# Performance work log

Hardware: AMD Instinct MI355X
Metric: run time of the kernel (lower is better)

Reference implementation:

```python
import jax, jax.numpy as jnp
import numpy as np
from jax import lax

MID = 64      # mid_size -> token seq len = MID*MID = 4096
DM = 64       # d_model = in_channels
DI = 128      # d_inner = expand * d_model
DS = 16       # d_state
DC = 4        # d_conv
DTR = 4       # dt_rank = ceil(DM/16)
EPS = 1e-5


def conv3x3(x, w):
    return lax.conv_general_dilated(x, w, (1, 1), ((1, 1), (1, 1)),
                                    dimension_numbers=('NCHW', 'OIHW', 'NCHW'))


def layernorm(x, w, b):
    mu = jnp.mean(x, -1, keepdims=True)
    var = jnp.mean((x - mu) ** 2, -1, keepdims=True)
    return (x - mu) * lax.rsqrt(var + EPS) * w + b


def bilinear(x, h, w):
    b, c = x.shape[:2]
    return jax.image.resize(x, (b, c, h, w), method='bilinear', antialias=False)


def mamba(tok, in_w, conv_w, conv_b, xproj_w, dt_w, dt_b, Alog, D, out_w):
    # tok: (b, L, DM)
    b, L, _ = tok.shape
    xz = tok @ in_w.T                                # (b, L, 2*DI)
    xc, z = jnp.split(xz, 2, axis=-1)
    # causal depthwise conv1d over sequence
    xcT = xc.transpose(0, 2, 1)                      # (b, DI, L)
    xconv = lax.conv_general_dilated(xcT, conv_w, (1,), ((DC - 1, 0),),
                                     dimension_numbers=('NCH', 'OIH', 'NCH'),
                                     feature_group_count=DI)
    xconv = xconv + conv_b[None, :, None]
    u = jax.nn.silu(xconv.transpose(0, 2, 1))        # (b, L, DI)
    x_dbl = u @ xproj_w.T                            # (b, L, DTR+2*DS)
    dt, B, C = jnp.split(x_dbl, [DTR, DTR + DS], axis=-1)
    dt = jax.nn.softplus(dt @ dt_w.T + dt_b)         # (b, L, DI)
    A = -jnp.exp(Alog)                               # (DI, DS)
    dA = jnp.exp(dt[..., None] * A)                  # (b, L, DI, DS)
    dBu = dt[..., None] * B[:, :, None, :] * u[..., None]

    def step(h, xs):
        a_t, bu_t = xs
        h = a_t * h + bu_t
        return h, h

    h0 = jnp.zeros((b, DI, DS), dt.dtype)
    _, hs = lax.scan(step, h0, (dA.transpose(1, 0, 2, 3), dBu.transpose(1, 0, 2, 3)))
    y = jnp.einsum('lbns,bls->bln', hs, C) + u * D   # (b, L, DI)
    y = y * jax.nn.silu(z)
    return y @ out_w.T                               # (b, L, DM)


def setup_inputs() -> dict:
    key = jax.random.key(0)
    ks = iter(jax.random.split(key, 32))
    s = 0.02
    d = {}
    d['x'] = jax.random.normal(next(ks), (4, 64, 128, 128), jnp.float32)
    for n, shp in [('cb_w1', (64, 64, 3, 3)), ('cb_w2', (64, 64, 3, 3)),
                   ('sm_w1', (64, 64, 3, 3)), ('sm_w2', (64, 64, 3, 3))]:
        d[n] = jax.random.normal(next(ks), shp, jnp.float32) * s
    d['ln1_w'] = jnp.ones((DM,), jnp.float32); d['ln1_b'] = jnp.zeros((DM,), jnp.float32)
    d['ln2_w'] = jnp.ones((DM,), jnp.float32); d['ln2_b'] = jnp.zeros((DM,), jnp.float32)
    for p in ['m1', 'm2']:
        d[p + '_in_w'] = jax.random.normal(next(ks), (2 * DI, DM), jnp.float32) * s
        d[p + '_conv_w'] = jax.random.normal(next(ks), (DI, 1, DC), jnp.float32) * s
        d[p + '_conv_b'] = jnp.zeros((DI,), jnp.float32)
        d[p + '_xproj_w'] = jax.random.normal(next(ks), (DTR + 2 * DS, DI), jnp.float32) * s
        d[p + '_dt_w'] = jax.random.normal(next(ks), (DI, DTR), jnp.float32) * s
        d[p + '_dt_b'] = jnp.full((DI,), -2.0, jnp.float32)
        d[p + '_Alog'] = jnp.broadcast_to(jnp.log(jnp.arange(1, DS + 1, dtype=jnp.float32)), (DI, DS)).copy()
        d[p + '_D'] = jnp.ones((DI,), jnp.float32)
        d[p + '_out_w'] = jax.random.normal(next(ks), (DM, DI), jnp.float32) * s
    return d


def reference(x, cb_w1, cb_w2, ln1_w, ln1_b, ln2_w, ln2_b,
              m1_in_w, m1_conv_w, m1_conv_b, m1_xproj_w, m1_dt_w, m1_dt_b, m1_Alog, m1_D, m1_out_w,
              m2_in_w, m2_conv_w, m2_conv_b, m2_xproj_w, m2_dt_w, m2_dt_b, m2_Alog, m2_D, m2_out_w,
              sm_w1, sm_w2):
    b, c, h, w = x.shape
    xr = conv3x3(jax.nn.relu(conv3x3(x, cb_w1)), cb_w2) + x
    x_small = xr if (h, w) == (MID, MID) else bilinear(xr, MID, MID)
    tokens = x_small.reshape(b, c, MID * MID).transpose(0, 2, 1)   # (b, L, c)
    main = mamba(layernorm(tokens, ln1_w, ln1_b),
                 m1_in_w, m1_conv_w, m1_conv_b, m1_xproj_w, m1_dt_w, m1_dt_b, m1_Alog, m1_D, m1_out_w)
    gate_feat = mamba(layernorm(tokens, ln2_w, ln2_b),
                      m2_in_w, m2_conv_w, m2_conv_b, m2_xproj_w, m2_dt_w, m2_dt_b, m2_Alog, m2_D, m2_out_w)
    gate = jax.nn.softmax(gate_feat, axis=1)                       # softmax over token dim
    tokens = tokens + gate * main
    feat = tokens.transpose(0, 2, 1).reshape(b, c, MID, MID)
    if (h, w) != (MID, MID):
        feat = bilinear(feat, h, w)
    return conv3x3(jax.nn.relu(conv3x3(feat, sm_w1)), sm_w2)
```

## Files before the change

### kernel.cpp

```cpp
#include <hip/hip_runtime.h>

typedef unsigned int u32;
typedef unsigned short u16;
typedef __attribute__((ext_vector_type(8))) short short8;
typedef __attribute__((ext_vector_type(4))) float f32x4;

__device__ __forceinline__ float sigmoidf_(float x){
  return 1.f / (1.f + __expf(-x));
}
__device__ __forceinline__ u16 f2bf(float f){
  union { float f; u32 i; } v; v.f = f;
  u32 r = v.i + 0x7fffu + ((v.i >> 16) & 1u);
  return (u16)(r >> 16);
}
__device__ __forceinline__ float bf2f(u32 u){
  union { float f; u32 i; } v; v.i = (u & 0xffffu) << 16; return v.f;
}
__device__ __forceinline__ float softplus_(float x){
  return fmaxf(x, 0.f) + __logf(1.f + __expf(-fabsf(x)));
}

__global__ void k_wswz2b(const float* __restrict__ wA, u16* __restrict__ WHA, u16* __restrict__ WLA,
                         const float* __restrict__ wB, u16* __restrict__ WHB, u16* __restrict__ WLB,
                         u16* __restrict__ BPH, u16* __restrict__ BPL){
  int gidx = blockIdx.x * 256 + threadIdx.x;
  if (gidx < 73728){
    int sel = gidx >= 36864;
    int idx = gidx - sel * 36864;
    const float* w = sel ? wB : wA;
    u16* WH = sel ? WHB : WHA;
    u16* WL = sel ? WLB : WLA;
    int j    = idx & 7;
    int lane = (idx >> 3) & 63;
    int nt   = (idx >> 9) & 3;
    int kc   = (idx >> 11) & 1;
    int t    = idx >> 12;
    int ic = kc * 32 + ((lane >> 4) & 3) * 8 + j;
    int oc = nt * 16 + (lane & 15);
    float v = w[(oc * 64 + ic) * 9 + t];
    u16 h = f2bf(v);
    u16 l = f2bf(v - bf2f(h));
    WH[idx] = h; WL[idx] = l;
  } else {
    int i = gidx - 73728;
    if (i >= 2064) return;
    int b = i / 516, p = i - b * 516;
    int y, x;
    if (p < 130){ y = 0; x = p; }
    else if (p < 260){ y = 129; x = p - 130; }
    else if (p < 388){ y = p - 260 + 1; x = 0; }
    else { y = p - 388 + 1; x = 129; }
    size_t o = (((size_t)b * 130 + y) * 130 + x) * 64;
    uint4 z = make_uint4(0, 0, 0, 0);
#pragma unroll
    for (int q = 0; q < 8; q++){
      *(uint4*)(BPH + o + q * 8) = z;
      *(uint4*)(BPL + o + q * 8) = z;
    }
  }
}

__global__ __launch_bounds__(256) void k_prep(const float* __restrict__ src,
                                              u16* __restrict__ PH, u16* __restrict__ PL){
  __shared__ float ld[64 * 129];
  int yp = blockIdx.x;
  int b  = blockIdx.y;
  int ys = yp - 1;
  int tid = threadIdx.x;
  if ((u32)ys < 128u){
    for (int i = tid; i < 8192; i += 256){
      int c = i >> 7, x = i & 127;
      ld[c * 129 + x] = src[((size_t)(b * 64 + c) * 128 + ys) * 128 + x];
    }
  }
  __syncthreads();
  for (int i = tid; i < 130 * 64; i += 256){
    int xp = i >> 6, c = i & 63;
    float v = 0.f;
    if ((u32)ys < 128u && (u32)(xp - 1) < 128u) v = ld[c * 129 + (xp - 1)];
    u16 h = f2bf(v);
    u16 l = f2bf(v - bf2f(h));
    size_t o = (((size_t)b * 130 + yp) * 130 + xp) * 64 + c;
    PH[o] = h; PL[o] = l;
  }
}

__global__ __launch_bounds__(256) void k_prepup(const float* __restrict__ FEAT,
                                                u16* __restrict__ PH, u16* __restrict__ PL){
  __shared__ float ld0[64 * 65], ld1[64 * 65];
  int yp = blockIdx.x;
  int b  = blockIdx.y;
  int ys = yp - 1;
  int tid = threadIdx.x;
  float wy = 0.f;
  if ((u32)ys < 128u){
    float ay = 0.5f * ys - 0.25f;
    int fy = (int)floorf(ay); wy = ay - fy;
    int y0s = fy < 0 ? 0 : fy, y1s = fy + 1 > 63 ? 63 : fy + 1;
    for (int i = tid; i < 1024; i += 256){
      int c = i >> 4, x4 = (i & 15) * 4;
      float4 a0 = *(const float4*)&FEAT[((size_t)(b * 64 + c) * 64 + y0s) * 64 + x4];
      float4 a1 = *(const float4*)&FEAT[((size_t)(b * 64 + c) * 64 + y1s) * 64 + x4];
      ld0[c * 65 + x4 + 0] = a0.x; ld0[c * 65 + x4 + 1] = a0.y;
      ld0[c * 65 + x4 + 2] = a0.z; ld0[c * 65 + x4 + 3] = a0.w;
      ld1[c * 65 + x4 + 0] = a1.x; ld1[c * 65 + x4 + 1] = a1.y;
      ld1[c * 65 + x4 + 2] = a1.z; ld1[c * 65 + x4 + 3] = a1.w;
    }
  }
  __syncthreads();
  for (int i = tid; i < 130 * 64; i += 256){
    int xp = i >> 6, c = i & 63;
    float v = 0.f;
    int xs = xp - 1;
    if ((u32)ys < 128u && (u32)xs < 128u){
      float ax = 0.5f * xs - 0.25f;
      int fx = (int)floorf(ax); float wx = ax - fx;
      int x0s = fx < 0 ? 0 : fx, x1s = fx + 1 > 63 ? 63 : fx + 1;
      float v0 = (1.f - wx) * ld0[c * 65 + x0s] + wx * ld0[c * 65 + x1s];
      float v1 = (1.f - wx) * ld1[c * 65 + x0s] + wx * ld1[c * 65 + x1s];
      v = (1.f - wy) * v0 + wy * v1;
    }
    u16 h = f2bf(v);
    u16 l = f2bf(v - bf2f(h));
    size_t o = (((size_t)b * 130 + yp) * 130 + xp) * 64 + c;
    PH[o] = h; PL[o] = l;
  }
}

__global__ __launch_bounds__(256) void k_convm(
    const u16* __restrict__ PH, const u16* __restrict__ PL,
    const u16* __restrict__ WH, const u16* __restrict__ WL,
    const float* __restrict__ resid,
    u16* __restrict__ OBH, u16* __restrict__ OBL,
    float* __restrict__ OUTF, float* __restrict__ T, float* __restrict__ NT,
    int mode)
{
  __shared__ __align__(16) u32 smem[17344];
  u16* Ah_s = (u16*)smem;
  u16* Al_s = Ah_s + 10368;
  int tid = threadIdx.x;
  int lane = tid & 63, w = tid >> 6;
  int quad = lane >> 4, lcol = lane & 15;
  int b = blockIdx.z, y0 = blockIdx.y * 16, x0 = blockIdx.x * 16;

  f32x4 acc[4][4];
#pragma unroll
  for (int mt = 0; mt < 4; mt++)
#pragma unroll
    for (int nt = 0; nt < 4; nt++)
      acc[mt][nt] = (f32x4){0.f, 0.f, 0.f, 0.f};

  for (int kc = 0; kc < 2; kc++){
    __syncthreads();
    for (int i = tid; i < 1296; i += 256){
      int q = i & 3;
      int rc = i >> 2;
      int r = rc / 18, c = rc - r * 18;
      size_t so = (((size_t)b * 130 + y0 + r) * 130 + (x0 + c)) * 64 + kc * 32 + q * 8;
      int de = rc * 32 + q * 8;
      *(uint4*)(Ah_s + de) = *(const uint4*)(PH + so);
      *(uint4*)(Al_s + de) = *(const uint4*)(PL + so);
    }
    __syncthreads();
#pragma unroll
    for (int t = 0; t < 9; t++){
      int dy = t / 3, dx = t - dy * 3;
      short8 bh[4], bl[4];
#pragma unroll
      for (int nt = 0; nt < 4; nt++){
        int o = ((t * 2 + kc) * 4 + nt) * 512 + lane * 8;
        bh[nt] = *(const short8*)(WH + o);
        bl[nt] = *(const short8*)(WL + o);
      }
      short8 ah[4], al[4];
#pragma unroll
      for (int mt = 0; mt < 4; mt++){
        int e = ((w * 4 + mt + dy) * 18 + (lcol + dx)) * 32 + quad * 8;
        ah[mt] = *(const short8*)(Ah_s + e);
        al[mt] = *(const short8*)(Al_s + e);
      }
#pragma unroll
      for (int mt = 0; mt < 4; mt++)
#pragma unroll
        for (int nt = 0; nt < 4; nt++){
          acc[mt][nt] = __builtin_amdgcn_mfma_f32_16x16x32_bf16(ah[mt], bh[nt], acc[mt][nt], 0, 0, 0);
          acc[mt][nt] = __builtin_amdgcn_mfma_f32_16x16x32_bf16(ah[mt], bl[nt], acc[mt][nt], 0, 0, 0);
          acc[mt][nt] = __builtin_amdgcn_mfma_f32_16x16x32_bf16(al[mt], bh[nt], acc[mt][nt], 0, 0, 0);
        }
    }
  }

  __syncthreads();
  if (mode == 0){
    u32* epi = smem;
#pragma unroll
    for (int mt = 0; mt < 4; mt++){
      int row = w * 4 + mt;
#pragma unroll
      for (int nt = 0; nt < 4; nt++){
#pragma unroll
        for (int reg = 0; reg < 4; reg++){
          float v = fmaxf(acc[mt][nt][reg], 0.f);
          u32 h = f2bf(v);
          u32 l = f2bf(v - bf2f(h));
          int ccol = quad * 4 + reg;
          int oc = nt * 16 + lcol;
          epi[(row * 16 + ccol) * 66 + oc] = h | (l << 16);
        }
      }
    }
    __syncthreads();
    for (int i = tid; i < 16384; i += 256){
      int px = i >> 6, oc = i & 63;
      int row = px >> 4, ccol = px & 15;
      u32 pk = epi[px * 66 + oc];
      size_t o = (((size_t)b * 130 + y0 + row + 1) * 130 + (x0 + ccol + 1)) * 64 + oc;
      OBH[o] = (u16)pk;
      OBL[o] = (u16)(pk >> 16);
    }
  } else {
    float* epi = (float*)smem;
#pragma unroll
    for (int mt = 0; mt < 4; mt++){
      int row = w * 4 + mt;
#pragma unroll
      for (int nt = 0; nt < 4; nt++){
#pragma unroll
        for (int reg = 0; reg < 4; reg++){
          int px = row * 16 + quad * 4 + reg;
          int oc = nt * 16 + lcol;
          epi[oc * 259 + px] = acc[mt][nt][reg];
        }
      }
    }
    __syncthreads();
    if (mode == 1){
      for (int i = tid; i < 16384; i += 256){
        int oc = i >> 8, px = i & 255;
        int row = px >> 4, c = px & 15;
        size_t o = (((size_t)b * 64 + oc) * 128 + y0 + row) * 128 + x0 + c;
        float v = epi[oc * 259 + px];
        if (resid) v += resid[o];
        OUTF[o] = v;
      }
    } else {
      for (int i = tid; i < 16384; i += 256){
        int oc = i >> 8, px = i & 255;
        int row = px >> 4, c = px & 15;
        size_t o = (((size_t)b * 64 + oc) * 128 + y0 + row) * 128 + x0 + c;
        epi[oc * 259 + px] += resid[o];
      }
      __syncthreads();
      float* redS  = (float*)smem + 16576;
      float* redQ  = redS + 320;
      float* stats = redQ + 320;
      int token = tid & 63, cg2 = tid >> 6;
      int tr = token >> 3, tc = token & 7;
      float av[16]; float s = 0.f, q = 0.f;
      int p0 = (2 * tr) * 16 + 2 * tc;
#pragma unroll
      for (int j = 0; j < 16; j++){
        int c = cg2 * 16 + ((j + tr) & 15);
        const float* ep = epi + c * 259;
        float v = 0.25f * (ep[p0] + ep[p0 + 1] + ep[p0 + 16] + ep[p0 + 17]);
        av[j] = v; s += v; q = fmaf(v, v, q);
      }
      redS[token * 5 + cg2] = s;
      redQ[token * 5 + cg2] = q;
      __syncthreads();
      if (tid < 64){
        float S = 0.f, Q = 0.f;
        for (int g = 0; g < 4; g++){ S += redS[tid * 5 + g]; Q += redQ[tid * 5 + g]; }
        float mu = S * (1.f / 64.f);
        float var = Q * (1.f / 64.f) - mu * mu;
        stats[tid * 2] = mu;
        stats[tid * 2 + 1] = rsqrtf(var + 1e-5f);
      }
      __syncthreads();
      float mu = stats[token * 2], inv = stats[token * 2 + 1];
      int l = (blockIdx.y * 8 + tr) * 64 + blockIdx.x * 8 + tc;
      size_t to = ((size_t)b * 4096 + l) * 64;
#pragma unroll
      for (int j = 0; j < 16; j++){
        int c = cg2 * 16 + ((j + tr) & 15);
        T[to + c] = av[j];
        NT[to + c] = (av[j] - mu) * inv;
      }
    }
  }
}

__global__ __launch_bounds__(256) void k_fold2(
    const float* __restrict__ Wa, const float* __restrict__ lnwa, const float* __restrict__ lnba,
    float* __restrict__ W2a, float* __restrict__ B2a,
    const float* __restrict__ Wb, const float* __restrict__ lnwb, const float* __restrict__ lnbb,
    float* __restrict__ W2b, float* __restrict__ B2b){
  int m = blockIdx.x;
  const float* W   = m ? Wb   : Wa;
  const float* lnw = m ? lnwb : lnwa;
  const float* lnb = m ? lnbb : lnba;
  float* W2 = m ? W2b : W2a;
  float* B2 = m ? B2b : B2a;
  __shared__ float gw[64], gb[64];
  int j = threadIdx.x;
  if (j < 64){ gw[j] = lnw[j]; gb[j] = lnb[j]; }
  __syncthreads();
  float bias = 0.f;
#pragma unroll
  for (int k4 = 0; k4 < 16; k4++){
    float4 wv = *(const float4*)&W[j * 64 + k4 * 4];
    W2[j * 64 + k4 * 4 + 0] = wv.x * gw[k4 * 4 + 0];
    W2[j * 64 + k4 * 4 + 1] = wv.y * gw[k4 * 4 + 1];
    W2[j * 64 + k4 * 4 + 2] = wv.z * gw[k4 * 4 + 2];
    W2[j * 64 + k4 * 4 + 3] = wv.w * gw[k4 * 4 + 3];
    bias = fmaf(wv.x, gb[k4 * 4 + 0], bias);
    bias = fmaf(wv.y, gb[k4 * 4 + 1], bias);
    bias = fmaf(wv.z, gb[k4 * 4 + 2], bias);
    bias = fmaf(wv.w, gb[k4 * 4 + 3], bias);
  }
  B2[j] = bias;
}

__global__ __launch_bounds__(256) void k_inprojdw(
    const float* __restrict__ NT,
    const float* __restrict__ W2a, const float* __restrict__ B2a,
    float* __restrict__ Ua, float* __restrict__ Za,
    const float* __restrict__ cwa, const float* __restrict__ cba,
    const float* __restrict__ W2b, const float* __restrict__ B2b,
    float* __restrict__ Ub, float* __restrict__ Zb,
    const float* __restrict__ cwb, const float* __restrict__ cbb)
{
  __shared__ float wL[64 * 68];
  __shared__ float xcs[67 * 68];
  int mz = blockIdx.z;
  const float* W2 = mz ? W2b : W2a;
  const float* B2 = mz ? B2b : B2a;
  float* U = mz ? Ub : Ua;
  float* Z  = mz ? Zb : Za;
  const float* cw = mz ? cwb : cwa;
  const float* cb = mz ? cbb : cba;
  int tid = threadIdx.x;
  int t0 = blockIdx.x * 64;
  int j0 = blockIdx.y * 64;
  for (int i = tid; i < 4096; i += 256){
    int jl = i >> 6, k = i & 63;
    wL[jl * 68 + k] = W2[(size_t)(j0 + jl) * 64 + k];
  }
  __syncthreads();
  int tq = tid >> 4, cg = tid & 15;
  const float* ntp = NT + (size_t)(t0 + tq * 4) * 64;
  float acc[4][4];
#pragma unroll
  for (int c = 0; c < 4; c++){
    float bias = B2[j0 + cg + c * 16];
#pragma unroll
    for (int t = 0; t < 4; t++) acc[t][c] = bias;
  }
#pragma unroll 4
  for (int k4 = 0; k4 < 16; k4++){
    float4 lv[4];
#pragma unroll
    for (int t = 0; t < 4; t++)
      lv[t] = *(const float4*)(ntp + t * 64 + k4 * 4);
    float4 wv[4];
#pragma unroll
    for (int c = 0; c < 4; c++)
      wv[c] = *(const float4*)&wL[(cg + c * 16) * 68 + k4 * 4];
#pragma unroll
    for (int t = 0; t < 4; t++)
#pragma unroll
      for (int c = 0; c < 4; c++){
        acc[t][c] = fmaf(lv[t].x, wv[c].x, acc[t][c]);
        acc[t][c] = fmaf(lv[t].y, wv[c].y, acc[t][c]);
        acc[t][c] = fmaf(lv[t].z, wv[c].z, acc[t][c]);
        acc[t][c] = fmaf(lv[t].w, wv[c].w, acc[t][c]);
      }
  }
  if (j0 < 128){
    int isStart = ((t0 & 4095) == 0);
    if (tid < 192){
      int e = tid >> 6, col = tid & 63;
      float v = 0.f;
      if (!isStart){
        const float* np = NT + (size_t)(t0 - 3 + e) * 64;
        float a2 = B2[j0 + col];
#pragma unroll 4
        for (int k = 0; k < 64; k += 4){
          float4 nv = *(const float4*)(np + k);
          float4 wv = *(const float4*)&wL[col * 68 + k];
          a2 = fmaf(nv.x, wv.x, fmaf(nv.y, wv.y, fmaf(nv.z, wv.z, fmaf(nv.w, wv.w, a2))));
        }
        v = a2;
      }
      xcs[e * 68 + col] = v;
    }
#pragma unroll
    for (int t = 0; t < 4; t++)
#pragma unroll
      for (int c = 0; c < 4; c++)
        xcs[(3 + tq * 4 + t) * 68 + cg + c * 16] = acc[t][c];
    __syncthreads();
#pragma unroll
    for (int c = 0; c < 4; c++){
      int lc = cg + c * 16;
      int ch = j0 + lc;
      float4 wv = *(const float4*)(cw + ch * 4);
      float bias = cb[ch];
#pragma unroll
      for (int t = 0; t < 4; t++){
        int row = 3 + tq * 4 + t;
        float a = bias;
        a = fmaf(wv.w, xcs[row * 68 + lc], a);
        a = fmaf(wv.z, xcs[(row - 1) * 68 + lc], a);
        a = fmaf(wv.y, xcs[(row - 2) * 68 + lc], a);
        a = fmaf(wv.x, xcs[(row - 3) * 68 + lc], a);
        size_t tg = t0 + tq * 4 + t;
        U[tg * 128 + ch] = a * sigmoidf_(a);
      }
    }
  } else {
#pragma unroll
    for (int t = 0; t < 4; t++){
      size_t tg = t0 + tq * 4 + t;
#pragma unroll
      for (int c = 0; c < 4; c++)
        Z[tg * 128 + (j0 - 128) + cg + c * 16] = acc[t][c];
    }
  }
}

__global__ __launch_bounds__(256) void k_xprojdt(
    const float* __restrict__ U0, const float* __restrict__ XW0, float* __restrict__ DBL0,
    const float* __restrict__ U1, const float* __restrict__ XW1, float* __restrict__ DBL1)
{
  __shared__ float xw[36 * 132];
  int bid = blockIdx.x;
  int m = bid >> 7, blk = bid & 127;
  const float* Up   = m ? U1   : U0;
  const float* XWp  = m ? XW1  : XW0;
  float* DBLp = m ? DBL1 : DBL0;
  int tid = threadIdx.x;
  for (int i = tid; i < 4608; i += 256)
    xw[(i >> 7) * 132 + (i & 127)] = XWp[i];
  __syncthreads();
  int slot = tid >> 2, jq = tid & 3;
  size_t tgA = (size_t)blk * 128 + slot;
  size_t tgB = tgA + 64;
  const float4* upA = (const float4*)(Up + tgA * 128);
  const float4* upB = (const float4*)(Up + tgB * 128);
  float accA[9], accB[9];
#pragma unroll
  for (int jj = 0; jj < 9; jj++){ accA[jj] = 0.f; accB[jj] = 0.f; }
  for (int k4 = 0; k4 < 32; k4++){
    float4 uA = upA[k4];
    float4 uB = upB[k4];
#pragma unroll
    for (int jj = 0; jj < 9; jj++){
      float4 w = *(const float4*)&xw[(jq * 9 + jj) * 132 + k4 * 4];
      accA[jj] = fmaf(w.x, uA.x, fmaf(w.y, uA.y, fmaf(w.z, uA.z, fmaf(w.w, uA.w, accA[jj]))));
      accB[jj] = fmaf(w.x, uB.x, fmaf(w.y, uB.y, fmaf(w.z, uB.z, fmaf(w.w, uB.w, accB[jj]))));
    }
  }
#pragma unroll
  for (int jj = 0; jj < 9; jj++){
    DBLp[tgA * 36 + jq * 9 + jj] = accA[jj];
    DBLp[tgB * 36 + jq * 9 + jj] = accB[jj];
  }
}

__global__ __launch_bounds__(256) void k_scanA(
    const float* __restrict__ DBL0, const float* __restrict__ U0, const float* __restrict__ AL0,
    const float* __restrict__ DTW0, const float* __restrict__ DTB0,
    const float* __restrict__ DBL1, const float* __restrict__ U1, const float* __restrict__ AL1,
    const float* __restrict__ DTW1, const float* __restrict__ DTB1,
    float* __restrict__ HF, float* __restrict__ AP)
{
  __shared__ float su[64 * 65], sB[16 * 68], sdtr[256];
  int bid = blockIdx.x;
  int cg = bid & 1;
  int c  = (bid >> 1) & 63;
  int b  = (bid >> 7) & 3;
  int m  = bid >> 9;
  const float* DBLp = m ? DBL1 : DBL0;
  const float* Up   = m ? U1   : U0;
  const float* ALp  = m ? AL1  : AL0;
  const float* DTWp = m ? DTW1 : DTW0;
  const float* DTBp = m ? DTB1 : DTB0;
  int tid = threadIdx.x;
  int lane = tid & 63, w = tid >> 6;
  int lcol = lane & 15, q = lane >> 4;
  int chL = w * 16 + lcol;
  int n = cg * 64 + chL;
  size_t base = (size_t)b * 4096 + c * 64;
  for (int i = tid; i < 4096; i += 256){
    int ch = i & 63, l = i >> 6;
    su[l * 65 + ch] = Up[(base + l) * 128 + cg * 64 + ch];
  }
  for (int i = tid; i < 1024; i += 256){
    int s = i & 15, l = i >> 4;
    sB[s * 68 + l] = DBLp[(base + l) * 36 + 4 + s];
  }
  {
    int l = tid >> 2, jj = tid & 3;
    sdtr[tid] = DBLp[(base + l) * 36 + jj];
  }
  const float LOG2E = 1.4426950408889634f;
  float A1[4];
#pragma unroll
  for (int j = 0; j < 4; j++) A1[j] = -__expf(ALp[n * 16 + q * 4 + j]) * LOG2E;
  float4 wdt = *(const float4*)(DTWp + n * 4);
  float bdt = DTBp[n];
  __syncthreads();
  float h[4] = {0.f, 0.f, 0.f, 0.f};
  float ap[4] = {1.f, 1.f, 1.f, 1.f};
#pragma unroll
  for (int l4 = 0; l4 < 16; l4++){
    float4 Bv[4];
#pragma unroll
    for (int j = 0; j < 4; j++) Bv[j] = *(const float4*)&sB[(q * 4 + j) * 68 + l4 * 4];
#pragma unroll
    for (int jj = 0; jj < 4; jj++){
      int l = l4 * 4 + jj;
      float4 d = *(const float4*)&sdtr[l * 4];
      float x = bdt;
      x = fmaf(wdt.x, d.x, x); x = fmaf(wdt.y, d.y, x);
      x = fmaf(wdt.z, d.z, x); x = fmaf(wdt.w, d.w, x);
      float dt = softplus_(x);
      float u  = su[l * 65 + chL];
      float dtu = dt * u;
#pragma unroll
      for (int j = 0; j < 4; j++){
        float a = exp2f(dt * A1[j]);
        h[j] = fmaf(a, h[j], dtu * (&Bv[j].x)[jj]);
        ap[j] *= a;
      }
    }
  }
  size_t o = ((size_t)((m * 4 + b) * 64 + c)) * 2048 + n * 16 + q * 4;
  *(float4*)&HF[o] = make_float4(h[0], h[1], h[2], h[3]);
  *(float4*)&AP[o] = make_float4(ap[0], ap[1], ap[2], ap[3]);
}

__global__ __launch_bounds__(64) void k_scanB(
    const float* __restrict__ HF, const float* __restrict__ AP, float* __restrict__ HIN)
{
  int r = blockIdx.x * 64 + threadIdx.x;
  int q = r >> 11;
  int p = r & 2047;
  size_t base = (size_t)q * 64 * 2048 + p;
  float h = 0.f;
  for (int c8 = 0; c8 < 8; c8++){
    float a[8], f[8];
#pragma unroll
    for (int j = 0; j < 8; j++){
      size_t o = base + (size_t)(c8 * 8 + j) * 2048;
      a[j] = AP[o]; f[j] = HF[o];
    }
#pragma unroll
    for (int j = 0; j < 8; j++){
      size_t o = base + (size_t)(c8 * 8 + j) * 2048;
      HIN[o] = h;
      h = fmaf(a[j], h, f[j]);
    }
  }
}

__global__ __launch_bounds__(256) void k_scanC(
    const float* __restrict__ DBL0, const float* __restrict__ U0, const float* __restrict__ AL0,
    const float* __restrict__ DTW0, const float* __restrict__ DTB0,
    const float* __restrict__ D0, float* __restrict__ Y0,
    const float* __restrict__ DBL1, const float* __restrict__ U1, const float* __restrict__ AL1,
    const float* __restrict__ DTW1, const float* __restrict__ DTB1,
    const float* __restrict__ D1, float* __restrict__ Y1,
    const float* __restrict__ HIN)
{
  __shared__ float su[64 * 65], sB[16 * 68], sC[16 * 68], sdtr[256];
  int bid = blockIdx.x;
  int cg = bid & 1;
  int c  = (bid >> 1) & 63;
  int b  = (bid >> 7) & 3;
  int m  = bid >> 9;
  const float* DBLp = m ? DBL1 : DBL0;
  const float* Up   = m ? U1   : U0;
  const float* ALp  = m ? AL1  : AL0;
  const float* DTWp = m ? DTW1 : DTW0;
  const float* DTBp = m ? DTB1 : DTB0;
  const float* Dp   = m ? D1   : D0;
  float*       Yp   = m ? Y1   : Y0;
  int tid = threadIdx.x;
  int lane = tid & 63, w = tid >> 6;
  int lcol = lane & 15, q = lane >> 4;
  int chL = w * 16 + lcol;
  int n = cg * 64 + chL;
  size_t base = (size_t)b * 4096 + c * 64;
  for (int i = tid; i < 4096; i += 256){
    int ch = i & 63, l = i >> 6;
    su[l * 65 + ch] = Up[(base + l) * 128 + cg * 64 + ch];
  }
  for (int i = tid; i < 1024; i += 256){
    int s = i & 15, l = i >> 4;
    size_t ob = (base + l) * 36;
    sB[s * 68 + l] = DBLp[ob + 4 + s];
    sC[s * 68 + l] = DBLp[ob + 20 + s];
  }
  {
    int l = tid >> 2, jj = tid & 3;
    sdtr[tid] = DBLp[(base + l) * 36 + jj];
  }
  const float LOG2E = 1.4426950408889634f;
  float A1[4];
#pragma unroll
  for (int j = 0; j < 4; j++) A1[j] = -__expf(ALp[n * 16 + q * 4 + j]) * LOG2E;
  float4 wdt = *(const float4*)(DTWp + n * 4);
  float bdt = DTBp[n];
  float Dn = Dp[n];
  float4 hv = *(const float4*)&HIN[((size_t)((m * 4 + b) * 64 + c)) * 2048 + n * 16 + q * 4];
  float h[4] = {hv.x, hv.y, hv.z, hv.w};
  __syncthreads();
#pragma unroll
  for (int l4 = 0; l4 < 16; l4++){
    float4 Bv[4], Cv[4];
#pragma unroll
    for (int j = 0; j < 4; j++){
      Bv[j] = *(const float4*)&sB[(q * 4 + j) * 68 + l4 * 4];
      Cv[j] = *(const float4*)&sC[(q * 4 + j) * 68 + l4 * 4];
    }
#pragma unroll
    for (int jj = 0; jj < 4; jj++){
      int l = l4 * 4 + jj;
      float4 d = *(const float4*)&sdtr[l * 4];
      float x = bdt;
      x = fmaf(wdt.x, d.x, x); x = fmaf(wdt.y, d.y, x);
      x = fmaf(wdt.z, d.z, x); x = fmaf(wdt.w, d.w, x);
      float dt = softplus_(x);
      float u  = su[l * 65 + chL];
      float dtu = dt * u;
      float p = 0.f;
#pragma unroll
      for (int j = 0; j < 4; j++){
        float a = exp2f(dt * A1[j]);
        h[j] = fmaf(a, h[j], dtu * (&Bv[j].x)[jj]);
        p = fmaf(h[j], (&Cv[j].x)[jj], p);
      }
      p += __shfl_xor(p, 16);
      p += __shfl_xor(p, 32);
      if (q == 0)
        Yp[(base + l) * 128 + n] = fmaf(u, Dn, p);
    }
  }
}

__global__ __launch_bounds__(256) void k_outproj(
    const float* __restrict__ Y0, const float* __restrict__ Zg0,
    const float* __restrict__ W0, float* __restrict__ OUT0,
    const float* __restrict__ Y1, const float* __restrict__ Zg1,
    const float* __restrict__ W1, float* __restrict__ OUT1)
{
  __shared__ float yl[16 * 128];
  __shared__ float wT[128 * 65];
  int m = blockIdx.y;
  const float* Y  = m ? Y1  : Y0;
  const float* Zg = m ? Zg1 : Zg0;
  const float* W  = m ? W1  : W0;
  float* OUT = m ? OUT1 : OUT0;
  int tid = threadIdx.x;
  size_t t0 = (size_t)blockIdx.x * 16;
  for (int i = tid; i < 2048; i += 256){
    float z = Zg[t0 * 128 + i];
    yl[i] = Y[t0 * 128 + i] * (z * sigmoidf_(z));
  }
  for (int i = tid; i < 8192; i += 256){
    int k = i & 127, j = i >> 7;
    wT[k * 65 + j] = W[j * 128 + k];
  }
  __syncthreads();
  int j = tid & 63;
  int tg = tid >> 6;
  float acc[4] = {0.f, 0.f, 0.f, 0.f};
  for (int k = 0; k < 128; k += 4){
    float w0 = wT[k * 65 + j], w1 = wT[(k+1) * 65 + j];
    float w2 = wT[(k+2) * 65 + j], w3 = wT[(k+3) * 65 + j];
#pragma unroll
    for (int t = 0; t < 4; t++){
      float4 yv = *(const float4*)&yl[(tg * 4 + t) * 128 + k];
      acc[t] = fmaf(w0, yv.x, fmaf(w1, yv.y, fmaf(w2, yv.z, fmaf(w3, yv.w, acc[t]))));
    }
  }
#pragma unroll
  for (int t = 0; t < 4; t++)
    OUT[(t0 + tg * 4 + t) * 64 + j] = acc[t];
}

__global__ void k_smA(const float* __restrict__ G, float* __restrict__ P){
  int bid = blockIdx.x;
  int b = bid >> 6, lc = bid & 63;
  int tid = threadIdx.x;
  int j = tid & 63, part = tid >> 6;
  size_t base = (size_t)b * 4096 + lc * 64;
  float mx = -3.4e38f;
  for (int i = 0; i < 16; i++){
    int l = part + i * 4;
    mx = fmaxf(mx, G[(base + l) * 64 + j]);
  }
  float sm = 0.f;
  for (int i = 0; i < 16; i++){
    int l = part + i * 4;
    sm += __expf(G[(base + l) * 64 + j] - mx);
  }
  __shared__ float sM[256], sS[256];
  sM[tid] = mx; sS[tid] = sm;
  __syncthreads();
  if (tid < 64){
    float M = sM[tid], S = sS[tid];
    for (int p = 1; p < 4; p++){
      float m2 = sM[p * 64 + tid], s2 = sS[p * 64 + tid];
      float Mn = fmaxf(M, m2);
      S = S * __expf(M - Mn) + s2 * __expf(m2 - Mn);
      M = Mn;
    }
    P[(bid * 64 + tid) * 2] = M;
    P[(bid * 64 + tid) * 2 + 1] = S;
  }
}

__global__ void k_smB(const float* __restrict__ P, float* __restrict__ F){
  int tid = threadIdx.x;
  int b = tid >> 6, j = tid & 63;
  float M = -3.4e38f, S = 0.f;
  for (int lc = 0; lc < 64; lc++){
    int idx = ((b * 64 + lc) * 64 + j) * 2;
    float m2 = P[idx], s2 = P[idx + 1];
    float Mn = fmaxf(M, m2);
    S = S * __expf(M - Mn) + s2 * __expf(m2 - Mn);
    M = Mn;
  }
  F[(b * 64 + j) * 2] = M;
  F[(b * 64 + j) * 2 + 1] = S;
}

__global__ void k_combine(const float* __restrict__ T, const float* __restrict__ MAIN,
                          const float* __restrict__ G, const float* __restrict__ F,
                          float* __restrict__ FEAT){
  int bid = blockIdx.x;
  int b = bid >> 6, row = bid & 63;
  int tid = threadIdx.x;
  int j = tid & 63, ls = tid >> 6;
  __shared__ float tile[64 * 65];
  float M = F[(b * 64 + j) * 2], invS = 1.f / F[(b * 64 + j) * 2 + 1];
  size_t lbase = (size_t)b * 4096 + row * 64;
  for (int i = 0; i < 16; i++){
    int col = ls + i * 4;
    size_t off = (lbase + col) * 64 + j;
    float g = __expf(G[off] - M) * invS;
    tile[col * 65 + j] = T[off] + g * MAIN[off];
  }
  __syncthreads();
  int colw = tid & 63, jr = tid >> 6;
  for (int jj = jr; jj < 64; jj += 4)
    FEAT[(((size_t)b * 64 + jj) * 64 + row) * 64 + colw] = tile[colw * 65 + jj];
}

extern "C" void kernel_launch(void* const* d_in, const int* in_sizes, int n_in,
                              void* d_out, int out_size, void* d_ws, size_t ws_size,
                              hipStream_t stream) {
  const size_t P1A = 0, P1B = 4326400;
  const size_t MB0 = 0, MB1 = 10027008;
  const size_t O_LN = 0, O_XC = 1048576, O_Z = 3145728, O_U = 5242880,
               O_DBL = 9437184;
  const size_t TOK = 20054016, OUT0 = 21102592, OUT1 = 22151168;
  const size_t FEAT = 23208448;
  const size_t P3A = 4194304, P3B = 8520704;
  const size_t WA_H = 19000000, WA_L = 19018432, WB_H = 19036864, WB_L = 19055296;
  const size_t PADN = 2163200;
  const size_t SMP = 0, SMF = 65536;
  const size_t W2_0 = 21102592, B2_0 = 21118976, W2_1 = 21119232, B2_1 = 21135616;
  const size_t TOTAL = 24257024;
  if (ws_size < TOTAL * 4) return;

  float* ws = (float*)d_ws;
  const float* X   = (const float*)d_in[0];
  const float* CB1 = (const float*)d_in[1];
  const float* CB2 = (const float*)d_in[2];
  const float* SW1 = (const float*)d_in[3];
  const float* SW2 = (const float*)d_in[4];
  const float* LNW[2] = { (const float*)d_in[5], (const float*)d_in[7] };
  const float* LNB[2] = { (const float*)d_in[6], (const float*)d_in[8] };
  const float *INW[2], *CW[2], *CBb[2], *XPW[2], *DTW[2], *DTB[2], *AL[2], *DD[2], *OW[2];
  for (int m = 0; m < 2; m++){
    int p = 9 + m * 9;
    INW[m] = (const float*)d_in[p + 0];
    CW[m]  = (const float*)d_in[p + 1];
    CBb[m] = (const float*)d_in[p + 2];
    XPW[m] = (const float*)d_in[p + 3];
    DTW[m] = (const float*)d_in[p + 4];
    DTB[m] = (const float*)d_in[p + 5];
    AL[m]  = (const float*)d_in[p + 6];
    DD[m]  = (const float*)d_in[p + 7];
    OW[m]  = (const float*)d_in[p + 8];
  }

  u16* wah = (u16*)(ws + WA_H); u16* wal = (u16*)(ws + WA_L);
  u16* wbh = (u16*)(ws + WB_H); u16* wbl = (u16*)(ws + WB_L);

  {
    u16* pah = (u16*)(ws + P1A); u16* pal = pah + PADN * 2;
    u16* pbh = (u16*)(ws + P1B); u16* pbl = pbh + PADN * 2;
    k_wswz2b<<<297, 256, 0, stream>>>(CB1, wah, wal, CB2, wbh, wbl, pbh, pbl);
    k_prep<<<dim3(130, 4), 256, 0, stream>>>(X, pah, pal);
    k_convm<<<dim3(8, 8, 4), 256, 0, stream>>>(pah, pal, wah, wal, nullptr,
                                               pbh, pbl, nullptr, nullptr, nullptr, 0);
    k_convm<<<dim3(8, 8, 4), 256, 0, stream>>>(pbh, pbl, wbh, wbl, X,
                                               nullptr, nullptr, nullptr,
                                               ws + TOK, ws + MB0 + O_LN, 2);
  }

  k_fold2<<<2, 256, 0, stream>>>(INW[0], LNW[0], LNB[0], ws + W2_0, ws + B2_0,
                                 INW[1], LNW[1], LNB[1], ws + W2_1, ws + B2_1);
  k_inprojdw<<<dim3(256, 4, 2), 256, 0, stream>>>(
      ws + MB0 + O_LN,
      ws + W2_0, ws + B2_0, ws + MB0 + O_U, ws + MB0 + O_Z, CW[0], CBb[0],
      ws + W2_1, ws + B2_1, ws + MB1 + O_U, ws + MB1 + O_Z, CW[1], CBb[1]);
  k_xprojdt<<<256, 256, 0, stream>>>(
      ws + MB0 + O_U, XPW[0], ws + MB0 + O_DBL,
      ws + MB1 + O_U, XPW[1], ws + MB1 + O_DBL);

  float* HF  = ws + MB0 + O_XC;
  float* AP  = ws + MB0 + O_XC + 1048576;
  float* HIN = ws + MB0 + O_LN;

  k_scanA<<<1024, 256, 0, stream>>>(
      ws + MB0 + O_DBL, ws + MB0 + O_U, AL[0], DTW[0], DTB[0],
      ws + MB1 + O_DBL, ws + MB1 + O_U, AL[1], DTW[1], DTB[1],
      HF, AP);
  k_scanB<<<256, 64, 0, stream>>>(HF, AP, HIN);
  k_scanC<<<1024, 256, 0, stream>>>(
      ws + MB0 + O_DBL, ws + MB0 + O_U, AL[0], DTW[0], DTB[0], DD[0], ws + MB0 + O_XC,
      ws + MB1 + O_DBL, ws + MB1 + O_U, AL[1], DTW[1], DTB[1], DD[1], ws + MB1 + O_XC,
      HIN);

  k_outproj<<<dim3(1024, 2), 256, 0, stream>>>(
      ws + MB0 + O_XC, ws + MB0 + O_Z, OW[0], ws + OUT0,
      ws + MB1 + O_XC, ws + MB1 + O_Z, OW[1], ws + OUT1);

  k_smA<<<256, 256, 0, stream>>>(ws + OUT1, ws + SMP);
  k_smB<<<1, 256, 0, stream>>>(ws + SMP, ws + SMF);
  k_combine<<<256, 256, 0, stream>>>(ws + TOK, ws + OUT0, ws + OUT1, ws + SMF, ws + FEAT);

  {
    u16* pah = (u16*)(ws + P3A); u16* pal = pah + PADN * 2;
    u16* pbh = (u16*)(ws + P3B); u16* pbl = pbh + PADN * 2;
    k_wswz2b<<<297, 256, 0, stream>>>(SW1, wah, wal, SW2, wbh, wbl, pbh, pbl);
    k_prepup<<<dim3(130, 4), 256, 0, stream>>>(ws + FEAT, pah, pal);
    k_convm<<<dim3(8, 8, 4), 256, 0, stream>>>(pah, pal, wah, wal, nullptr,
                                               pbh, pbl, nullptr, nullptr, nullptr, 0);
    k_convm<<<dim3(8, 8, 4), 256, 0, stream>>>(pbh, pbl, wbh, wbl, nullptr,
                                               nullptr, nullptr, (float*)d_out,
                                               nullptr, nullptr, 1);
  }
}
```

Before: 397.0 us.

## Merge setup kernels, fold softmax reduction into combine, dedupe dt softplus in scan

All four conv weight swizzles and the LayerNorm-into-in_proj fold now run in one setup kernel. Border zeroing of the padded conv buffers moves into the prep kernels, and the single-block softmax-stats kernel is folded into the combine kernel, which recomputes the column max and sum per block. This cuts four launches and the serial 1-block stage. In the scan kernels each lane computes one dt softplus per 4 tokens and shares it by shuffle instead of recomputing it for every token, at the cost of redundant softmax-stat reads in every combine block.

```diff
diff --git a/kernel.cpp b/kernel.cpp
--- a/kernel.cpp
+++ b/kernel.cpp
@@ -20,16 +20,23 @@
   return fmaxf(x, 0.f) + __logf(1.f + __expf(-fabsf(x)));
 }
 
-__global__ void k_wswz2b(const float* __restrict__ wA, u16* __restrict__ WHA, u16* __restrict__ WLA,
-                         const float* __restrict__ wB, u16* __restrict__ WHB, u16* __restrict__ WLB,
-                         u16* __restrict__ BPH, u16* __restrict__ BPL){
+__global__ void k_setup(const float* __restrict__ w0, u16* __restrict__ h0, u16* __restrict__ l0,
+                        const float* __restrict__ w1, u16* __restrict__ h1, u16* __restrict__ l1,
+                        const float* __restrict__ w2, u16* __restrict__ h2, u16* __restrict__ l2,
+                        const float* __restrict__ w3, u16* __restrict__ h3, u16* __restrict__ l3,
+                        const float* __restrict__ Wa, const float* __restrict__ lnwa, const float* __restrict__ lnba,
+                        float* __restrict__ W2a, float* __restrict__ B2a,
+                        const float* __restrict__ Wb, const float* __restrict__ lnwb, const float* __restrict__ lnbb,
+                        float* __restrict__ W2b, float* __restrict__ B2b){
   int gidx = blockIdx.x * 256 + threadIdx.x;
-  if (gidx < 73728){
-    int sel = gidx >= 36864;
-    int idx = gidx - sel * 36864;
-    const float* w = sel ? wB : wA;
-    u16* WH = sel ? WHB : WHA;
-    u16* WL = sel ? WLB : WLA;
+  if (gidx < 147456){
+    int set = gidx / 36864;
+    int idx = gidx - set * 36864;
+    const float* w; u16* WH; u16* WL;
+    if (set == 0){ w = w0; WH = h0; WL = l0; }
+    else if (set == 1){ w = w1; WH = h1; WL = l1; }
+    else if (set == 2){ w = w2; WH = h2; WL = l2; }
+    else { w = w3; WH = h3; WL = l3; }
     int j    = idx & 7;
     int lane = (idx >> 3) & 63;
     int nt   = (idx >> 9) & 3;
@@ -42,31 +49,54 @@
     u16 l = f2bf(v - bf2f(h));
     WH[idx] = h; WL[idx] = l;
   } else {
-    int i = gidx - 73728;
-    if (i >= 2064) return;
-    int b = i / 516, p = i - b * 516;
-    int y, x;
-    if (p < 130){ y = 0; x = p; }
-    else if (p < 260){ y = 129; x = p - 130; }
-    else if (p < 388){ y = p - 260 + 1; x = 0; }
-    else { y = p - 388 + 1; x = 129; }
-    size_t o = (((size_t)b * 130 + y) * 130 + x) * 64;
-    uint4 z = make_uint4(0, 0, 0, 0);
-#pragma unroll
-    for (int q = 0; q < 8; q++){
-      *(uint4*)(BPH + o + q * 8) = z;
-      *(uint4*)(BPL + o + q * 8) = z;
-    }
+    int i = gidx - 147456;
+    if (i >= 128) return;
+    int m = i >> 6, j = i & 63;
+    const float* W   = m ? Wb   : Wa;
+    const float* lnw = m ? lnwb : lnwa;
+    const float* lnb = m ? lnbb : lnba;
+    float* W2 = m ? W2b : W2a;
+    float* B2 = m ? B2b : B2a;
+    float bias = 0.f;
+#pragma unroll
+    for (int k4 = 0; k4 < 16; k4++){
+      float4 wv = *(const float4*)&W[j * 64 + k4 * 4];
+      float4 gw = *(const float4*)&lnw[k4 * 4];
+      float4 gb = *(const float4*)&lnb[k4 * 4];
+      W2[j * 64 + k4 * 4 + 0] = wv.x * gw.x;
+      W2[j * 64 + k4 * 4 + 1] = wv.y * gw.y;
+      W2[j * 64 + k4 * 4 + 2] = wv.z * gw.z;
+      W2[j * 64 + k4 * 4 + 3] = wv.w * gw.w;
+      bias = fmaf(wv.x, gb.x, bias);
+      bias = fmaf(wv.y, gb.y, bias);
+      bias = fmaf(wv.z, gb.z, bias);
+      bias = fmaf(wv.w, gb.w, bias);
+    }
+    B2[j] = bias;
   }
 }
 
 __global__ __launch_bounds__(256) void k_prep(const float* __restrict__ src,
-                                              u16* __restrict__ PH, u16* __restrict__ PL){
+                                              u16* __restrict__ PH, u16* __restrict__ PL,
+                                              u16* __restrict__ BPH, u16* __restrict__ BPL){
   __shared__ float ld[64 * 129];
   int yp = blockIdx.x;
   int b  = blockIdx.y;
   int ys = yp - 1;
   int tid = threadIdx.x;
+  if (yp == 0 || yp == 129){
+    for (int i = tid; i < 130 * 64; i += 256){
+      int x = i >> 6, c = i & 63;
+      size_t o = (((size_t)b * 130 + yp) * 130 + x) * 64 + c;
+      BPH[o] = 0; BPL[o] = 0;
+    }
+  } else {
+    for (int i = tid; i < 128; i += 256){
+      int x = (i >= 64) ? 129 : 0, c = i & 63;
+      size_t o = (((size_t)b * 130 + yp) * 130 + x) * 64 + c;
+      BPH[o] = 0; BPL[o] = 0;
+    }
+  }
   if ((u32)ys < 128u){
     for (int i = tid; i < 8192; i += 256){
       int c = i >> 7, x = i & 127;
@@ -86,12 +116,26 @@
 }
 
 __global__ __launch_bounds__(256) void k_prepup(const float* __restrict__ FEAT,
-                                                u16* __restrict__ PH, u16* __restrict__ PL){
+                                                u16* __restrict__ PH, u16* __restrict__ PL,
+                                                u16* __restrict__ BPH, u16* __restrict__ BPL){
   __shared__ float ld0[64 * 65], ld1[64 * 65];
   int yp = blockIdx.x;
   int b  = blockIdx.y;
   int ys = yp - 1;
   int tid = threadIdx.x;
+  if (yp == 0 || yp == 129){
+    for (int i = tid; i < 130 * 64; i += 256){
+      int x = i >> 6, c = i & 63;
+      size_t o = (((size_t)b * 130 + yp) * 130 + x) * 64 + c;
+      BPH[o] = 0; BPL[o] = 0;
+    }
+  } else {
+    for (int i = tid; i < 128; i += 256){
+      int x = (i >= 64) ? 129 : 0, c = i & 63;
+      size_t o = (((size_t)b * 130 + yp) * 130 + x) * 64 + c;
+      BPH[o] = 0; BPL[o] = 0;
+    }
+  }
   float wy = 0.f;
   if ((u32)ys < 128u){
     float ay = 0.5f * ys - 0.25f;
@@ -288,37 +332,6 @@
       }
     }
   }
-}
-
-__global__ __launch_bounds__(256) void k_fold2(
-    const float* __restrict__ Wa, const float* __restrict__ lnwa, const float* __restrict__ lnba,
-    float* __restrict__ W2a, float* __restrict__ B2a,
-    const float* __restrict__ Wb, const float* __restrict__ lnwb, const float* __restrict__ lnbb,
-    float* __restrict__ W2b, float* __restrict__ B2b){
-  int m = blockIdx.x;
-  const float* W   = m ? Wb   : Wa;
-  const float* lnw = m ? lnwb : lnwa;
-  const float* lnb = m ? lnbb : lnba;
-  float* W2 = m ? W2b : W2a;
-  float* B2 = m ? B2b : B2a;
-  __shared__ float gw[64], gb[64];
-  int j = threadIdx.x;
-  if (j < 64){ gw[j] = lnw[j]; gb[j] = lnb[j]; }
-  __syncthreads();
-  float bias = 0.f;
-#pragma unroll
-  for (int k4 = 0; k4 < 16; k4++){
-    float4 wv = *(const float4*)&W[j * 64 + k4 * 4];
-    W2[j * 64 + k4 * 4 + 0] = wv.x * gw[k4 * 4 + 0];
-    W2[j * 64 + k4 * 4 + 1] = wv.y * gw[k4 * 4 + 1];
-    W2[j * 64 + k4 * 4 + 2] = wv.z * gw[k4 * 4 + 2];
-    W2[j * 64 + k4 * 4 + 3] = wv.w * gw[k4 * 4 + 3];
-    bias = fmaf(wv.x, gb[k4 * 4 + 0], bias);
-    bias = fmaf(wv.y, gb[k4 * 4 + 1], bias);
-    bias = fmaf(wv.z, gb[k4 * 4 + 2], bias);
-    bias = fmaf(wv.w, gb[k4 * 4 + 3], bias);
-  }
-  B2[j] = bias;
 }
 
 __global__ __launch_bounds__(256) void k_inprojdw(
@@ -515,17 +528,24 @@
   float ap[4] = {1.f, 1.f, 1.f, 1.f};
 #pragma unroll
   for (int l4 = 0; l4 < 16; l4++){
+    int lq = l4 * 4 + q;
+    float4 dq = *(const float4*)&sdtr[lq * 4];
+    float xq = bdt;
+    xq = fmaf(wdt.x, dq.x, xq); xq = fmaf(wdt.y, dq.y, xq);
+    xq = fmaf(wdt.z, dq.z, xq); xq = fmaf(wdt.w, dq.w, xq);
+    float dtq = softplus_(xq);
+    float dts[4];
+    dts[0] = __shfl(dtq, lcol);
+    dts[1] = __shfl(dtq, lcol + 16);
+    dts[2] = __shfl(dtq, lcol + 32);
+    dts[3] = __shfl(dtq, lcol + 48);
     float4 Bv[4];
 #pragma unroll
     for (int j = 0; j < 4; j++) Bv[j] = *(const float4*)&sB[(q * 4 + j) * 68 + l4 * 4];
 #pragma unroll
     for (int jj = 0; jj < 4; jj++){
       int l = l4 * 4 + jj;
-      float4 d = *(const float4*)&sdtr[l * 4];
-      float x = bdt;
-      x = fmaf(wdt.x, d.x, x); x = fmaf(wdt.y, d.y, x);
-      x = fmaf(wdt.z, d.z, x); x = fmaf(wdt.w, d.w, x);
-      float dt = softplus_(x);
+      float dt = dts[jj];
       float u  = su[l * 65 + chL];
       float dtu = dt * u;
 #pragma unroll
@@ -619,6 +639,17 @@
   __syncthreads();
 #pragma unroll
   for (int l4 = 0; l4 < 16; l4++){
+    int lq = l4 * 4 + q;
+    float4 dq = *(const float4*)&sdtr[lq * 4];
+    float xq = bdt;
+    xq = fmaf(wdt.x, dq.x, xq); xq = fmaf(wdt.y, dq.y, xq);
+    xq = fmaf(wdt.z, dq.z, xq); xq = fmaf(wdt.w, dq.w, xq);
+    float dtq = softplus_(xq);
+    float dts[4];
+    dts[0] = __shfl(dtq, lcol);
+    dts[1] = __shfl(dtq, lcol + 16);
+    dts[2] = __shfl(dtq, lcol + 32);
+    dts[3] = __shfl(dtq, lcol + 48);
     float4 Bv[4], Cv[4];
 #pragma unroll
     for (int j = 0; j < 4; j++){
@@ -628,11 +659,7 @@
 #pragma unroll
     for (int jj = 0; jj < 4; jj++){
       int l = l4 * 4 + jj;
-      float4 d = *(const float4*)&sdtr[l * 4];
-      float x = bdt;
-      x = fmaf(wdt.x, d.x, x); x = fmaf(wdt.y, d.y, x);
-      x = fmaf(wdt.z, d.z, x); x = fmaf(wdt.w, d.w, x);
-      float dt = softplus_(x);
+      float dt = dts[jj];
       float u  = su[l * 65 + chL];
       float dtu = dt * u;
       float p = 0.f;
@@ -723,30 +750,41 @@
   }
 }
 
-__global__ void k_smB(const float* __restrict__ P, float* __restrict__ F){
-  int tid = threadIdx.x;
-  int b = tid >> 6, j = tid & 63;
-  float M = -3.4e38f, S = 0.f;
-  for (int lc = 0; lc < 64; lc++){
-    int idx = ((b * 64 + lc) * 64 + j) * 2;
-    float m2 = P[idx], s2 = P[idx + 1];
-    float Mn = fmaxf(M, m2);
-    S = S * __expf(M - Mn) + s2 * __expf(m2 - Mn);
-    M = Mn;
-  }
-  F[(b * 64 + j) * 2] = M;
-  F[(b * 64 + j) * 2 + 1] = S;
-}
-
 __global__ void k_combine(const float* __restrict__ T, const float* __restrict__ MAIN,
-                          const float* __restrict__ G, const float* __restrict__ F,
+                          const float* __restrict__ G, const float* __restrict__ P,
                           float* __restrict__ FEAT){
   int bid = blockIdx.x;
   int b = bid >> 6, row = bid & 63;
   int tid = threadIdx.x;
+  __shared__ float tile[64 * 65];
+  __shared__ float sM[256], sS[256], Mv[64], iSv[64];
+  {
+    int j2 = tid & 63, part = tid >> 6;
+    float M = -3.4e38f, S = 0.f;
+    for (int i = 0; i < 16; i++){
+      int lc = part + i * 4;
+      int idx = ((b * 64 + lc) * 64 + j2) * 2;
+      float m2 = P[idx], s2 = P[idx + 1];
+      float Mn = fmaxf(M, m2);
+      S = S * __expf(M - Mn) + s2 * __expf(m2 - Mn);
+      M = Mn;
+    }
+    sM[tid] = M; sS[tid] = S;
+  }
+  __syncthreads();
+  if (tid < 64){
+    float M = sM[tid], S = sS[tid];
+    for (int p = 1; p < 4; p++){
+      float m2 = sM[p * 64 + tid], s2 = sS[p * 64 + tid];
+      float Mn = fmaxf(M, m2);
+      S = S * __expf(M - Mn) + s2 * __expf(m2 - Mn);
+      M = Mn;
+    }
+    Mv[tid] = M; iSv[tid] = 1.f / S;
+  }
+  __syncthreads();
   int j = tid & 63, ls = tid >> 6;
-  __shared__ float tile[64 * 65];
-  float M = F[(b * 64 + j) * 2], invS = 1.f / F[(b * 64 + j) * 2 + 1];
+  float M = Mv[j], invS = iSv[j];
   size_t lbase = (size_t)b * 4096 + row * 64;
   for (int i = 0; i < 16; i++){
     int col = ls + i * 4;
@@ -770,9 +808,9 @@
   const size_t TOK = 20054016, OUT0 = 21102592, OUT1 = 22151168;
   const size_t FEAT = 23208448;
   const size_t P3A = 4194304, P3B = 8520704;
-  const size_t WA_H = 19000000, WA_L = 19018432, WB_H = 19036864, WB_L = 19055296;
+  const size_t WSET = 19000000;
   const size_t PADN = 2163200;
-  const size_t SMP = 0, SMF = 65536;
+  const size_t SMP = 0;
   const size_t W2_0 = 21102592, B2_0 = 21118976, W2_1 = 21119232, B2_1 = 21135616;
   const size_t TOTAL = 24257024;
   if (ws_size < TOTAL * 4) return;
@@ -799,23 +837,26 @@
     OW[m]  = (const float*)d_in[p + 8];
   }
 
-  u16* wah = (u16*)(ws + WA_H); u16* wal = (u16*)(ws + WA_L);
-  u16* wbh = (u16*)(ws + WB_H); u16* wbl = (u16*)(ws + WB_L);
-
-  {
-    u16* pah = (u16*)(ws + P1A); u16* pal = pah + PADN * 2;
-    u16* pbh = (u16*)(ws + P1B); u16* pbl = pbh + PADN * 2;
-    k_wswz2b<<<297, 256, 0, stream>>>(CB1, wah, wal, CB2, wbh, wbl, pbh, pbl);
-    k_prep<<<dim3(130, 4), 256, 0, stream>>>(X, pah, pal);
-    k_convm<<<dim3(8, 8, 4), 256, 0, stream>>>(pah, pal, wah, wal, nullptr,
-                                               pbh, pbl, nullptr, nullptr, nullptr, 0);
-    k_convm<<<dim3(8, 8, 4), 256, 0, stream>>>(pbh, pbl, wbh, wbl, X,
-                                               nullptr, nullptr, nullptr,
-                                               ws + TOK, ws + MB0 + O_LN, 2);
-  }
-
-  k_fold2<<<2, 256, 0, stream>>>(INW[0], LNW[0], LNB[0], ws + W2_0, ws + B2_0,
-                                 INW[1], LNW[1], LNB[1], ws + W2_1, ws + B2_1);
+  u16* wset[8];
+  for (int k = 0; k < 8; k++) wset[k] = (u16*)(ws + WSET + (size_t)k * 18432);
+
+  u16* p1ah = (u16*)(ws + P1A); u16* p1al = p1ah + PADN * 2;
+  u16* p1bh = (u16*)(ws + P1B); u16* p1bl = p1bh + PADN * 2;
+  u16* p3ah = (u16*)(ws + P3A); u16* p3al = p3ah + PADN * 2;
+  u16* p3bh = (u16*)(ws + P3B); u16* p3bl = p3bh + PADN * 2;
+
+  k_setup<<<577, 256, 0, stream>>>(CB1, wset[0], wset[1], CB2, wset[2], wset[3],
+                                   SW1, wset[4], wset[5], SW2, wset[6], wset[7],
+                                   INW[0], LNW[0], LNB[0], ws + W2_0, ws + B2_0,
+                                   INW[1], LNW[1], LNB[1], ws + W2_1, ws + B2_1);
+
+  k_prep<<<dim3(130, 4), 256, 0, stream>>>(X, p1ah, p1al, p1bh, p1bl);
+  k_convm<<<dim3(8, 8, 4), 256, 0, stream>>>(p1ah, p1al, wset[0], wset[1], nullptr,
+                                             p1bh, p1bl, nullptr, nullptr, nullptr, 0);
+  k_convm<<<dim3(8, 8, 4), 256, 0, stream>>>(p1bh, p1bl, wset[2], wset[3], X,
+                                             nullptr, nullptr, nullptr,
+                                             ws + TOK, ws + MB0 + O_LN, 2);
+
   k_inprojdw<<<dim3(256, 4, 2), 256, 0, stream>>>(
       ws + MB0 + O_LN,
       ws + W2_0, ws + B2_0, ws + MB0 + O_U, ws + MB0 + O_Z, CW[0], CBb[0],
@@ -843,18 +884,12 @@
       ws + MB1 + O_XC, ws + MB1 + O_Z, OW[1], ws + OUT1);
 
   k_smA<<<256, 256, 0, stream>>>(ws + OUT1, ws + SMP);
-  k_smB<<<1, 256, 0, stream>>>(ws + SMP, ws + SMF);
-  k_combine<<<256, 256, 0, stream>>>(ws + TOK, ws + OUT0, ws + OUT1, ws + SMF, ws + FEAT);
-
-  {
-    u16* pah = (u16*)(ws + P3A); u16* pal = pah + PADN * 2;
-    u16* pbh = (u16*)(ws + P3B); u16* pbl = pbh + PADN * 2;
-    k_wswz2b<<<297, 256, 0, stream>>>(SW1, wah, wal, SW2, wbh, wbl, pbh, pbl);
-    k_prepup<<<dim3(130, 4), 256, 0, stream>>>(ws + FEAT, pah, pal);
-    k_convm<<<dim3(8, 8, 4), 256, 0, stream>>>(pah, pal, wah, wal, nullptr,
-                                               pbh, pbl, nullptr, nullptr, nullptr, 0);
-    k_convm<<<dim3(8, 8, 4), 256, 0, stream>>>(pbh, pbl, wbh, wbl, nullptr,
-                                               nullptr, nullptr, (float*)d_out,
-                                               nullptr, nullptr, 1);
-  }
-}
+  k_combine<<<256, 256, 0, stream>>>(ws + TOK, ws + OUT0, ws + OUT1, ws + SMP, ws + FEAT);
+
+  k_prepup<<<dim3(130, 4), 256, 0, stream>>>(ws + FEAT, p3ah, p3al, p3bh, p3bl);
+  k_convm<<<dim3(8, 8, 4), 256, 0, stream>>>(p3ah, p3al, wset[4], wset[5], nullptr,
+                                             p3bh, p3bl, nullptr, nullptr, nullptr, 0);
+  k_convm<<<dim3(8, 8, 4), 256, 0, stream>>>(p3bh, p3bl, wset[6], wset[7], nullptr,
+                                             nullptr, nullptr, (float*)d_out,
+                                             nullptr, nullptr, 1);
+}
```

Measured after the change: 377.5 us. 4.9% less time.
